# Kernel tuning notes

Hardware: AMD Instinct MI355X
Metric: run time of the kernel (lower is better)

Reference implementation:

```python
import jax, jax.numpy as jnp
import numpy as np

TOP_K = 6
N_EXPERTS = 64
N_GROUP = 8
TOPK_GROUP = 3
HIDDEN = 2048


def setup_inputs() -> dict:
    key = jax.random.key(0)
    kx, kw = jax.random.split(key)
    x = jax.random.normal(kx, (4, 4096, HIDDEN), dtype=jnp.float32)
    # kaiming_uniform_(a=sqrt(5)) on [N_EXPERTS, HIDDEN]: bound = 1/sqrt(fan_in)
    bound = 1.0 / np.sqrt(HIDDEN)
    weight = jax.random.uniform(kw, (N_EXPERTS, HIDDEN), dtype=jnp.float32,
                                minval=-bound, maxval=bound)
    return {"x": x, "weight": weight}


def reference(x, weight):
    b, s, h = x.shape
    tokens = b * s
    hs = x.reshape(tokens, h).astype(jnp.float32)
    logits = hs @ weight.astype(jnp.float32).T          # [T, E]
    scores = jax.nn.softmax(logits, axis=-1)            # [T, E]

    # group-limited greedy routing
    epg = N_EXPERTS // N_GROUP                          # experts per group
    group_scores = scores.reshape(tokens, N_GROUP, epg).max(axis=-1)  # [T, G]
    _, group_idx = jax.lax.top_k(group_scores, TOPK_GROUP)            # [T, Kg]
    group_mask = jnp.zeros((tokens, N_GROUP), dtype=scores.dtype)
    group_mask = group_mask.at[jnp.arange(tokens)[:, None], group_idx].set(1.0)
    score_mask = jnp.repeat(group_mask, epg, axis=-1)   # [T, E]
    tmp_scores = jnp.where(score_mask > 0, scores, 0.0)
    topk_weight, topk_idx = jax.lax.top_k(tmp_scores, TOP_K)  # [T, K]
    return topk_idx, topk_weight
```

## Files before the change

kernel.cpp:

```cpp
#include <hip/hip_runtime.h>
#include <math.h>

#define TOKENS 16384
#define HIDDEN 2048
#define NEXP   64
#define MBLK   64
#define KBLK   16
#define NWAVE  4
#define KCH    (HIDDEN / NWAVE)
#define NTILE  (KCH / KBLK)
#define TOPK   6
#define NGROUP 8
#define TOPKG  3

__global__ __launch_bounds__(256, 1)
void moe_gate_kernel(const float* __restrict__ X, const float* __restrict__ W,
                     float* __restrict__ out, int half_out)
{
    __shared__ float xs[NWAVE][MBLK][KBLK + 1];
    __shared__ float wl[NWAVE][NEXP][KBLK + 1];
    __shared__ float red[MBLK][NEXP + 1];

    const int tid  = threadIdx.x;
    const int wv   = tid >> 6;
    const int lane = tid & 63;
    const int lr   = lane >> 3;
    const int lc   = lane & 7;
    const int row0 = blockIdx.x * MBLK;
    const int kb0  = wv * KCH;

    const int sr = lane >> 2;
    const int sc = lane & 3;

    float acc[8][8];
#pragma unroll
    for (int i = 0; i < 8; ++i)
#pragma unroll
        for (int j = 0; j < 8; ++j) acc[i][j] = 0.f;

    const float* xb = X + (size_t)row0 * HIDDEN + kb0;
    const float* wb = W + kb0;

    float4 px[4], pw[4];

#pragma unroll
    for (int it = 0; it < 4; ++it) {
        int r = it * 16 + sr;
        px[it] = *(const float4*)(xb + (size_t)r * HIDDEN + sc * 4);
        pw[it] = *(const float4*)(wb + (size_t)r * HIDDEN + sc * 4);
    }

    for (int t = 0; t < NTILE; ++t) {
#pragma unroll
        for (int it = 0; it < 4; ++it) {
            int r = it * 16 + sr;
            float* dx = &xs[wv][r][sc * 4];
            dx[0] = px[it].x; dx[1] = px[it].y; dx[2] = px[it].z; dx[3] = px[it].w;
            float* dw = &wl[wv][r][sc * 4];
            dw[0] = pw[it].x; dw[1] = pw[it].y; dw[2] = pw[it].z; dw[3] = pw[it].w;
        }
        __syncthreads();

        if (t + 1 < NTILE) {
            const float* xt = xb + (t + 1) * KBLK;
            const float* wt = wb + (t + 1) * KBLK;
#pragma unroll
            for (int it = 0; it < 4; ++it) {
                int r = it * 16 + sr;
                px[it] = *(const float4*)(xt + (size_t)r * HIDDEN + sc * 4);
                pw[it] = *(const float4*)(wt + (size_t)r * HIDDEN + sc * 4);
            }
        }

#pragma unroll 4
        for (int kk = 0; kk < KBLK; ++kk) {
            float a[8], b[8];
#pragma unroll
            for (int i = 0; i < 8; ++i) a[i] = xs[wv][i * 8 + lr][kk];
#pragma unroll
            for (int j = 0; j < 8; ++j) b[j] = wl[wv][j * 8 + lc][kk];
#pragma unroll
            for (int i = 0; i < 8; ++i)
#pragma unroll
                for (int j = 0; j < 8; ++j)
                    acc[i][j] = fmaf(a[i], b[j], acc[i][j]);
        }
        __syncthreads();
    }

    if (wv == 0) {
#pragma unroll
        for (int i = 0; i < 8; ++i)
#pragma unroll
            for (int j = 0; j < 8; ++j)
                red[i * 8 + lr][j * 8 + lc] = acc[i][j];
    }
    __syncthreads();
    for (int v = 1; v < NWAVE; ++v) {
        if (wv == v) {
#pragma unroll
            for (int i = 0; i < 8; ++i)
#pragma unroll
                for (int j = 0; j < 8; ++j)
                    red[i * 8 + lr][j * 8 + lc] += acc[i][j];
        }
        __syncthreads();
    }

    if (tid < MBLK) {
        const int t = tid;
        float s[NEXP];
        float m = -INFINITY;
#pragma unroll
        for (int e = 0; e < NEXP; ++e) { s[e] = red[t][e]; m = fmaxf(m, s[e]); }
        float sum = 0.f;
#pragma unroll
        for (int e = 0; e < NEXP; ++e) { s[e] = __expf(s[e] - m); sum += s[e]; }
        float inv = 1.f / sum;
#pragma unroll
        for (int e = 0; e < NEXP; ++e) s[e] *= inv;

        float gs[NGROUP];
#pragma unroll
        for (int g = 0; g < NGROUP; ++g) {
            float gm = s[g * 8];
#pragma unroll
            for (int q = 1; q < 8; ++q) gm = fmaxf(gm, s[g * 8 + q]);
            gs[g] = gm;
        }
        unsigned gmask = 0;
        for (int r = 0; r < TOPKG; ++r) {
            int bg = 0; float bv = -INFINITY;
#pragma unroll
            for (int g = 0; g < NGROUP; ++g) {
                bool avail = !((gmask >> g) & 1);
                if (avail && gs[g] > bv) { bv = gs[g]; bg = g; }
            }
            gmask |= 1u << bg;
        }
        unsigned long long chosen = 0ull;
        const int tok = row0 + t;
        for (int k = 0; k < TOPK; ++k) {
            int be = 0; float bv = -INFINITY;
#pragma unroll
            for (int e = 0; e < NEXP; ++e) {
                float v = ((gmask >> (e >> 3)) & 1u) ? s[e] : 0.f;
                bool avail = !((chosen >> e) & 1ull);
                if (avail && v > bv) { bv = v; be = e; }
            }
            chosen |= 1ull << be;
            out[(size_t)tok * TOPK + k] = (float)be;
            out[(size_t)half_out + (size_t)tok * TOPK + k] = bv;
        }
    }
}

extern "C" void kernel_launch(void* const* d_in, const int* in_sizes, int n_in,
                              void* d_out, int out_size, void* d_ws, size_t ws_size,
                              hipStream_t stream)
{
    const float* x = (const float*)d_in[0];
    const float* w = (const float*)d_in[1];
    float* out = (float*)d_out;
    const int half_out = out_size / 2;

    dim3 grid(TOKENS / MBLK);
    dim3 block(256);
    moe_gate_kernel<<<grid, block, 0, stream>>>(x, w, out, half_out);
}
```

Measured before the change: 104.0 us.

## Shrink token tile to 16 rows, raise occupancy, vectorize LDS reads

Cuts the per-block token tile from 64 to 16 rows, so each thread holds a 2x8 accumulator instead of 8x8, and lets up to 4 blocks share a CU. It also pads the LDS rows to 20 floats so the inner k-loop can read float4 vectors, and lowers the X prefetch to one float4 per thread. The goal is more blocks in flight (1024 instead of 256) and fewer LDS instructions. In exchange, each block reloads the whole weight tile for only 16 tokens, which quadruples W traffic through L2/LDS per token and lowers the FMA-to-load ratio.

```diff
diff --git a/kernel.cpp b/kernel.cpp
--- a/kernel.cpp
+++ b/kernel.cpp
@@ -4,21 +4,22 @@
 #define TOKENS 16384
 #define HIDDEN 2048
 #define NEXP   64
-#define MBLK   64
+#define MBLK   16
 #define KBLK   16
 #define NWAVE  4
 #define KCH    (HIDDEN / NWAVE)
 #define NTILE  (KCH / KBLK)
+#define RPAD   20
 #define TOPK   6
 #define NGROUP 8
 #define TOPKG  3
 
-__global__ __launch_bounds__(256, 1)
+__global__ __launch_bounds__(256, 4)
 void moe_gate_kernel(const float* __restrict__ X, const float* __restrict__ W,
                      float* __restrict__ out, int half_out)
 {
-    __shared__ float xs[NWAVE][MBLK][KBLK + 1];
-    __shared__ float wl[NWAVE][NEXP][KBLK + 1];
+    __shared__ float xs[NWAVE][MBLK][RPAD];
+    __shared__ float wl[NWAVE][NEXP][RPAD];
     __shared__ float red[MBLK][NEXP + 1];
 
     const int tid  = threadIdx.x;
@@ -32,65 +33,73 @@
     const int sr = lane >> 2;
     const int sc = lane & 3;
 
-    float acc[8][8];
+    float acc[2][8];
 #pragma unroll
-    for (int i = 0; i < 8; ++i)
+    for (int i = 0; i < 2; ++i)
 #pragma unroll
         for (int j = 0; j < 8; ++j) acc[i][j] = 0.f;
 
     const float* xb = X + (size_t)row0 * HIDDEN + kb0;
     const float* wb = W + kb0;
 
-    float4 px[4], pw[4];
+    float4 px;
+    float4 pw[4];
 
+    px = *(const float4*)(xb + (size_t)sr * HIDDEN + sc * 4);
 #pragma unroll
     for (int it = 0; it < 4; ++it) {
         int r = it * 16 + sr;
-        px[it] = *(const float4*)(xb + (size_t)r * HIDDEN + sc * 4);
         pw[it] = *(const float4*)(wb + (size_t)r * HIDDEN + sc * 4);
     }
 
     for (int t = 0; t < NTILE; ++t) {
+        {
+            float* dx = &xs[wv][sr][sc * 4];
+            dx[0] = px.x; dx[1] = px.y; dx[2] = px.z; dx[3] = px.w;
 #pragma unroll
-        for (int it = 0; it < 4; ++it) {
-            int r = it * 16 + sr;
-            float* dx = &xs[wv][r][sc * 4];
-            dx[0] = px[it].x; dx[1] = px[it].y; dx[2] = px[it].z; dx[3] = px[it].w;
-            float* dw = &wl[wv][r][sc * 4];
-            dw[0] = pw[it].x; dw[1] = pw[it].y; dw[2] = pw[it].z; dw[3] = pw[it].w;
+            for (int it = 0; it < 4; ++it) {
+                float* dw = &wl[wv][it * 16 + sr][sc * 4];
+                dw[0] = pw[it].x; dw[1] = pw[it].y; dw[2] = pw[it].z; dw[3] = pw[it].w;
+            }
         }
         __syncthreads();
 
         if (t + 1 < NTILE) {
             const float* xt = xb + (t + 1) * KBLK;
             const float* wt = wb + (t + 1) * KBLK;
+            px = *(const float4*)(xt + (size_t)sr * HIDDEN + sc * 4);
 #pragma unroll
             for (int it = 0; it < 4; ++it) {
                 int r = it * 16 + sr;
-                px[it] = *(const float4*)(xt + (size_t)r * HIDDEN + sc * 4);
                 pw[it] = *(const float4*)(wt + (size_t)r * HIDDEN + sc * 4);
             }
         }
 
-#pragma unroll 4
-        for (int kk = 0; kk < KBLK; ++kk) {
-            float a[8], b[8];
 #pragma unroll
-            for (int i = 0; i < 8; ++i) a[i] = xs[wv][i * 8 + lr][kk];
+        for (int k4 = 0; k4 < KBLK / 4; ++k4) {
+            float4 a[2], b[8];
 #pragma unroll
-            for (int j = 0; j < 8; ++j) b[j] = wl[wv][j * 8 + lc][kk];
+            for (int i = 0; i < 2; ++i)
+                a[i] = *(const float4*)&xs[wv][i * 8 + lr][k4 * 4];
 #pragma unroll
-            for (int i = 0; i < 8; ++i)
+            for (int j = 0; j < 8; ++j)
+                b[j] = *(const float4*)&wl[wv][j * 8 + lc][k4 * 4];
 #pragma unroll
-                for (int j = 0; j < 8; ++j)
-                    acc[i][j] = fmaf(a[i], b[j], acc[i][j]);
+            for (int i = 0; i < 2; ++i)
+#pragma unroll
+                for (int j = 0; j < 8; ++j) {
+                    acc[i][j] = fmaf(a[i].x, b[j].x, acc[i][j]);
+                    acc[i][j] = fmaf(a[i].y, b[j].y, acc[i][j]);
+                    acc[i][j] = fmaf(a[i].z, b[j].z, acc[i][j]);
+                    acc[i][j] = fmaf(a[i].w, b[j].w, acc[i][j]);
+                }
         }
         __syncthreads();
     }
 
     if (wv == 0) {
 #pragma unroll
-        for (int i = 0; i < 8; ++i)
+        for (int i = 0; i < 2; ++i)
 #pragma unroll
             for (int j = 0; j < 8; ++j)
                 red[i * 8 + lr][j * 8 + lc] = acc[i][j];
@@ -99,7 +108,7 @@
     for (int v = 1; v < NWAVE; ++v) {
         if (wv == v) {
 #pragma unroll
-            for (int i = 0; i < 8; ++i)
+            for (int i = 0; i < 2; ++i)
 #pragma unroll
                 for (int j = 0; j < 8; ++j)
                     red[i * 8 + lr][j * 8 + lc] += acc[i][j];
```

After: 135.4 us. 1.3x slower.

## Restructure gate GEMM: per-lane token rows, W read via broadcast loads, 8 waves

Applied to the files above, without the earlier changes.

Each wave now owns one 512-wide K chunk and half of the experts, and each lane computes one token row against 32 experts. W is read directly from global memory with wave-uniform addresses, so the shared-memory staging of W goes away. X is staged per wave with only a waitcnt instead of block barriers, and the block grows to 512 threads with two blocks per CU. This removes the block-wide syncs and W LDS traffic, but it depends on uniform W loads being served efficiently by cache, and the X LDS reads by row may cause bank conflicts.

```diff
diff --git a/kernel.cpp b/kernel.cpp
--- a/kernel.cpp
+++ b/kernel.cpp
@@ -5,104 +5,104 @@
 #define HIDDEN 2048
 #define NEXP   64
 #define MBLK   64
+#define NCHUNK 4
+#define KCH    512
 #define KBLK   16
-#define NWAVE  4
-#define KCH    (HIDDEN / NWAVE)
 #define NTILE  (KCH / KBLK)
+#define EHALF  32
+#define XPAD   20
+#define RPAD   68
 #define TOPK   6
 #define NGROUP 8
 #define TOPKG  3
 
-__global__ __launch_bounds__(256, 1)
+__global__ __launch_bounds__(512, 2)
 void moe_gate_kernel(const float* __restrict__ X, const float* __restrict__ W,
                      float* __restrict__ out, int half_out)
 {
-    __shared__ float xs[NWAVE][MBLK][KBLK + 1];
-    __shared__ float wl[NWAVE][NEXP][KBLK + 1];
-    __shared__ float red[MBLK][NEXP + 1];
+    __shared__ float xs[8][MBLK][XPAD];
+    __shared__ float red[MBLK][RPAD];
 
-    const int tid  = threadIdx.x;
-    const int wv   = tid >> 6;
-    const int lane = tid & 63;
-    const int lr   = lane >> 3;
-    const int lc   = lane & 7;
-    const int row0 = blockIdx.x * MBLK;
-    const int kb0  = wv * KCH;
+    const int tid   = threadIdx.x;
+    const int wv    = __builtin_amdgcn_readfirstlane(tid >> 6);
+    const int lane  = tid & 63;
+    const int chunk = wv >> 1;
+    const int eh    = wv & 1;
+    const int e0    = eh * EHALF;
+    const int kb0   = chunk * KCH;
+    const int row0  = blockIdx.x * MBLK;
+
+    float acc[EHALF];
+#pragma unroll
+    for (int j = 0; j < EHALF; ++j) acc[j] = 0.f;
+
+    const float* xb = X + (size_t)row0 * HIDDEN + kb0;
 
     const int sr = lane >> 2;
     const int sc = lane & 3;
 
-    float acc[8][8];
+    float4 px[4];
 #pragma unroll
-    for (int i = 0; i < 8; ++i)
-#pragma unroll
-        for (int j = 0; j < 8; ++j) acc[i][j] = 0.f;
+    for (int it = 0; it < 4; ++it)
+        px[it] = *(const float4*)(xb + (size_t)(it * 16 + sr) * HIDDEN + sc * 4);
 
-    const float* xb = X + (size_t)row0 * HIDDEN + kb0;
-    const float* wb = W + kb0;
-
-    float4 px[4], pw[4];
-
-#pragma unroll
-    for (int it = 0; it < 4; ++it) {
-        int r = it * 16 + sr;
-        px[it] = *(const float4*)(xb + (size_t)r * HIDDEN + sc * 4);
-        pw[it] = *(const float4*)(wb + (size_t)r * HIDDEN + sc * 4);
-    }
-
+#pragma unroll 1
     for (int t = 0; t < NTILE; ++t) {
 #pragma unroll
         for (int it = 0; it < 4; ++it) {
-            int r = it * 16 + sr;
-            float* dx = &xs[wv][r][sc * 4];
-            dx[0] = px[it].x; dx[1] = px[it].y; dx[2] = px[it].z; dx[3] = px[it].w;
-            float* dw = &wl[wv][r][sc * 4];
-            dw[0] = pw[it].x; dw[1] = pw[it].y; dw[2] = pw[it].z; dw[3] = pw[it].w;
+            float* d = &xs[wv][it * 16 + sr][sc * 4];
+            d[0] = px[it].x; d[1] = px[it].y; d[2] = px[it].z; d[3] = px[it].w;
         }
-        __syncthreads();
+        asm volatile("s_waitcnt lgkmcnt(0)" ::: "memory");
 
         if (t + 1 < NTILE) {
             const float* xt = xb + (t + 1) * KBLK;
-            const float* wt = wb + (t + 1) * KBLK;
 #pragma unroll
-            for (int it = 0; it < 4; ++it) {
-                int r = it * 16 + sr;
-                px[it] = *(const float4*)(xt + (size_t)r * HIDDEN + sc * 4);
-                pw[it] = *(const float4*)(wt + (size_t)r * HIDDEN + sc * 4);
-            }
+            for (int it = 0; it < 4; ++it)
+                px[it] = *(const float4*)(xt + (size_t)(it * 16 + sr) * HIDDEN + sc * 4);
         }
 
-#pragma unroll 4
-        for (int kk = 0; kk < KBLK; ++kk) {
-            float a[8], b[8];
+        float4 xq[4];
 #pragma unroll
-            for (int i = 0; i < 8; ++i) a[i] = xs[wv][i * 8 + lr][kk];
+        for (int c = 0; c < 4; ++c)
+            xq[c] = *(const float4*)&xs[wv][lane][c * 4];
+
+        const float* wk = W + (size_t)kb0 + (size_t)t * KBLK;
 #pragma unroll
-            for (int j = 0; j < 8; ++j) b[j] = wl[wv][j * 8 + lc][kk];
-#pragma unroll
-            for (int i = 0; i < 8; ++i)
-#pragma unroll
-                for (int j = 0; j < 8; ++j)
-                    acc[i][j] = fmaf(a[i], b[j], acc[i][j]);
+        for (int j = 0; j < EHALF; ++j) {
+            const float4* wr = (const float4*)(wk + (size_t)(e0 + j) * HIDDEN);
+            float4 w0 = wr[0], w1 = wr[1], w2 = wr[2], w3 = wr[3];
+            float a = acc[j];
+            a = fmaf(xq[0].x, w0.x, a); a = fmaf(xq[0].y, w0.y, a);
+            a = fmaf(xq[0].z, w0.z, a); a = fmaf(xq[0].w, w0.w, a);
+            a = fmaf(xq[1].x, w1.x, a); a = fmaf(xq[1].y, w1.y, a);
+            a = fmaf(xq[1].z, w1.z, a); a = fmaf(xq[1].w, w1.w, a);
+            a = fmaf(xq[2].x, w2.x, a); a = fmaf(xq[2].y, w2.y, a);
+            a = fmaf(xq[2].z, w2.z, a); a = fmaf(xq[2].w, w2.w, a);
+            a = fmaf(xq[3].x, w3.x, a); a = fmaf(xq[3].y, w3.y, a);
+            a = fmaf(xq[3].z, w3.z, a); a = fmaf(xq[3].w, w3.w, a);
+            acc[j] = a;
         }
-        __syncthreads();
     }
 
-    if (wv == 0) {
+    __syncthreads();
+    if (chunk == 0) {
 #pragma unroll
-        for (int i = 0; i < 8; ++i)
-#pragma unroll
-            for (int j = 0; j < 8; ++j)
-                red[i * 8 + lr][j * 8 + lc] = acc[i][j];
+        for (int q = 0; q < EHALF / 4; ++q) {
+            float4 v = make_float4(acc[q * 4], acc[q * 4 + 1], acc[q * 4 + 2], acc[q * 4 + 3]);
+            *(float4*)&red[lane][e0 + q * 4] = v;
+        }
     }
     __syncthreads();
-    for (int v = 1; v < NWAVE; ++v) {
-        if (wv == v) {
+    for (int c = 1; c < NCHUNK; ++c) {
+        if (chunk == c) {
 #pragma unroll
-            for (int i = 0; i < 8; ++i)
-#pragma unroll
-                for (int j = 0; j < 8; ++j)
-                    red[i * 8 + lr][j * 8 + lc] += acc[i][j];
+            for (int q = 0; q < EHALF / 4; ++q) {
+                float4 r = *(const float4*)&red[lane][e0 + q * 4];
+                r.x += acc[q * 4];     r.y += acc[q * 4 + 1];
+                r.z += acc[q * 4 + 2]; r.w += acc[q * 4 + 3];
+                *(float4*)&red[lane][e0 + q * 4] = r;
+            }
         }
         __syncthreads();
     }
@@ -165,6 +165,6 @@
     const int half_out = out_size / 2;
 
     dim3 grid(TOKENS / MBLK);
-    dim3 block(256);
+    dim3 block(512);
     moe_gate_kernel<<<grid, block, 0, stream>>>(x, w, out, half_out);
 }
```

Result: slower. 173.0 us (+66.3%).

## Drop per-tile block barriers and vectorize LDS tile reads with float4

Applied to the files above, without the earlier changes.

Each wave stages its own private K-chunk in LDS, so the per-tile __syncthreads are removed and only a single barrier remains before the cross-wave reduction. LDS rows are padded to 20 floats so whole float4 stores and loads work, and the inner product consumes four k values per LDS read. The goal is to cut barrier stalls and LDS instruction count. Correctness now relies on wave-private buffers and intra-wave lockstep, with no fence between a tile's reads and the next tile's overwrite.

```diff
diff --git a/kernel.cpp b/kernel.cpp
--- a/kernel.cpp
+++ b/kernel.cpp
@@ -5,10 +5,12 @@
 #define HIDDEN 2048
 #define NEXP   64
 #define MBLK   64
+#define NCHUNK 4
+#define KCH    512
 #define KBLK   16
-#define NWAVE  4
-#define KCH    (HIDDEN / NWAVE)
 #define NTILE  (KCH / KBLK)
+#define XPAD   20
+#define RPAD   68
 #define TOPK   6
 #define NGROUP 8
 #define TOPKG  3
@@ -17,12 +19,12 @@
 void moe_gate_kernel(const float* __restrict__ X, const float* __restrict__ W,
                      float* __restrict__ out, int half_out)
 {
-    __shared__ float xs[NWAVE][MBLK][KBLK + 1];
-    __shared__ float wl[NWAVE][NEXP][KBLK + 1];
-    __shared__ float red[MBLK][NEXP + 1];
+    __shared__ float xs[NCHUNK][MBLK][XPAD];
+    __shared__ float ws[NCHUNK][NEXP][XPAD];
+    __shared__ float red[MBLK][RPAD];
 
     const int tid  = threadIdx.x;
-    const int wv   = tid >> 6;
+    const int wv   = __builtin_amdgcn_readfirstlane(tid >> 6);
     const int lane = tid & 63;
     const int lr   = lane >> 3;
     const int lc   = lane & 7;
@@ -42,52 +44,54 @@
     const float* wb = W + kb0;
 
     float4 px[4], pw[4];
-
 #pragma unroll
     for (int it = 0; it < 4; ++it) {
-        int r = it * 16 + sr;
-        px[it] = *(const float4*)(xb + (size_t)r * HIDDEN + sc * 4);
-        pw[it] = *(const float4*)(wb + (size_t)r * HIDDEN + sc * 4);
+        px[it] = *(const float4*)(xb + (size_t)(it * 16 + sr) * HIDDEN + sc * 4);
+        pw[it] = *(const float4*)(wb + (size_t)(it * 16 + sr) * HIDDEN + sc * 4);
     }
 
+#pragma unroll 1
     for (int t = 0; t < NTILE; ++t) {
 #pragma unroll
         for (int it = 0; it < 4; ++it) {
-            int r = it * 16 + sr;
-            float* dx = &xs[wv][r][sc * 4];
-            dx[0] = px[it].x; dx[1] = px[it].y; dx[2] = px[it].z; dx[3] = px[it].w;
-            float* dw = &wl[wv][r][sc * 4];
-            dw[0] = pw[it].x; dw[1] = pw[it].y; dw[2] = pw[it].z; dw[3] = pw[it].w;
+            *(float4*)&xs[wv][it * 16 + sr][sc * 4] = px[it];
+            *(float4*)&ws[wv][it * 16 + sr][sc * 4] = pw[it];
         }
-        __syncthreads();
 
         if (t + 1 < NTILE) {
             const float* xt = xb + (t + 1) * KBLK;
             const float* wt = wb + (t + 1) * KBLK;
 #pragma unroll
             for (int it = 0; it < 4; ++it) {
-                int r = it * 16 + sr;
-                px[it] = *(const float4*)(xt + (size_t)r * HIDDEN + sc * 4);
-                pw[it] = *(const float4*)(wt + (size_t)r * HIDDEN + sc * 4);
+                px[it] = *(const float4*)(xt + (size_t)(it * 16 + sr) * HIDDEN + sc * 4);
+                pw[it] = *(const float4*)(wt + (size_t)(it * 16 + sr) * HIDDEN + sc * 4);
             }
         }
 
-#pragma unroll 4
-        for (int kk = 0; kk < KBLK; ++kk) {
-            float a[8], b[8];
 #pragma unroll
-            for (int i = 0; i < 8; ++i) a[i] = xs[wv][i * 8 + lr][kk];
+        for (int k4 = 0; k4 < 4; ++k4) {
+            float4 a[8], b[8];
 #pragma unroll
-            for (int j = 0; j < 8; ++j) b[j] = wl[wv][j * 8 + lc][kk];
+            for (int i = 0; i < 8; ++i)
+                a[i] = *(const float4*)&xs[wv][i * 8 + lr][k4 * 4];
+#pragma unroll
+            for (int j = 0; j < 8; ++j)
+                b[j] = *(const float4*)&ws[wv][j * 8 + lc][k4 * 4];
 #pragma unroll
             for (int i = 0; i < 8; ++i)
 #pragma unroll
-                for (int j = 0; j < 8; ++j)
-                    acc[i][j] = fmaf(a[i], b[j], acc[i][j]);
+                for (int j = 0; j < 8; ++j) {
+                    float v = acc[i][j];
+                    v = fmaf(a[i].x, b[j].x, v);
+                    v = fmaf(a[i].y, b[j].y, v);
+                    v = fmaf(a[i].z, b[j].z, v);
+                    v = fmaf(a[i].w, b[j].w, v);
+                    acc[i][j] = v;
+                }
         }
-        __syncthreads();
     }
 
+    __syncthreads();
     if (wv == 0) {
 #pragma unroll
         for (int i = 0; i < 8; ++i)
@@ -96,8 +100,8 @@
                 red[i * 8 + lr][j * 8 + lc] = acc[i][j];
     }
     __syncthreads();
-    for (int v = 1; v < NWAVE; ++v) {
-        if (wv == v) {
+    for (int c = 1; c < NCHUNK; ++c) {
+        if (wv == c) {
 #pragma unroll
             for (int i = 0; i < 8; ++i)
 #pragma unroll
```

Measured after the change: 135.0 us. +29.8%, slower.
